# Kernel tuning notes

Measured on AMD Instinct MI355X. Metric: run time of the kernel, lower is better.

## Reference

```python
import jax, jax.numpy as jnp
import numpy as np

B, OBS, NH, LAT = 8192, 256, 2048, 128

def setup_inputs() -> dict:
    key = jax.random.key(0)
    k1, k2, k3, k4, k5, k6 = jax.random.split(key, 6)
    s1 = 1.0 / np.sqrt(OBS + NH)
    s2 = 1.0 / np.sqrt(NH)
    return {
        "x": jax.random.normal(k1, (B, OBS), dtype=jnp.float32),
        "h": jax.random.normal(k2, (B, NH), dtype=jnp.float32),
        "W_i2h": jax.random.normal(k3, (NH, OBS + NH), dtype=jnp.float32) * s1,
        "b_i2h": jax.random.normal(k4, (NH,), dtype=jnp.float32) * s1,
        "W_h2o": jax.random.normal(k5, (2 * LAT, NH), dtype=jnp.float32) * s2,
        "b_h2o": jax.random.normal(k6, (2 * LAT,), dtype=jnp.float32) * s2,
    }

def reference(x, h, W_i2h, b_i2h, W_h2o, b_h2o):
    # combined = cat((x, h), dim=1)  -> [B, OBS+NH]
    combined = jnp.concatenate([x, h], axis=1)
    # h_new = tanh(i2h(combined));  Linear is y = x @ W.T + b
    h_new = jnp.tanh(combined @ W_i2h.T + b_i2h)
    out = h_new @ W_h2o.T + b_h2o  # [B, 2*LAT]
    return (out, h_new)
```

## Files before the change

### kernel.cpp

```cpp
#include <hip/hip_runtime.h>
#include <hip/hip_bf16.h>
#include <cstdint>

using bf16 = __hip_bfloat16;
typedef __attribute__((ext_vector_type(8))) short short8;
typedef __attribute__((ext_vector_type(4))) float floatx4;

static constexpr int BATCH = 8192;
static constexpr int K1    = 2304;
static constexpr int N1    = 2048;
static constexpr int K2    = 2048;
static constexpr int N2    = 256;

__device__ __forceinline__ void gload_lds16(const void* g, void* l) {
  __builtin_amdgcn_global_load_lds(
      (const __attribute__((address_space(1))) void*)g,
      (__attribute__((address_space(3))) void*)l, 16, 0, 0);
}

__device__ __forceinline__ float fast_tanh(float x) {
  float e = __builtin_amdgcn_exp2f(x * 2.8853900817779268f);
  return 1.0f - 2.0f * __builtin_amdgcn_rcpf(e + 1.0f);
}

__device__ __forceinline__ short8 cvt8(const float* src) {
  float4 a = ((const float4*)src)[0];
  float4 b = ((const float4*)src)[1];
  union { short8 v; bf16 e[8]; } u;
  u.e[0] = __float2bfloat16(a.x); u.e[1] = __float2bfloat16(a.y);
  u.e[2] = __float2bfloat16(a.z); u.e[3] = __float2bfloat16(a.w);
  u.e[4] = __float2bfloat16(b.x); u.e[5] = __float2bfloat16(b.y);
  u.e[6] = __float2bfloat16(b.z); u.e[7] = __float2bfloat16(b.w);
  return u.v;
}

static constexpr int SEG0 = BATCH * (K1 / 8);
static constexpr int SEG1 = N1 * K1 / 8;
static constexpr int SEG2 = N2 * K2 / 8;
__global__ __launch_bounds__(256) void prep(
    const float* __restrict__ x, const float* __restrict__ h,
    const float* __restrict__ W1, const float* __restrict__ W2,
    bf16* __restrict__ comb, bf16* __restrict__ W1b, bf16* __restrict__ W2b) {
  int i = blockIdx.x * 256 + threadIdx.x;
  if (i < SEG0) {
    int row  = i / 288;
    int slot = i - row * 288;
    const float* src = (slot < 32) ? (x + (size_t)row * 256 + slot * 8)
                                   : (h + (size_t)row * 2048 + (slot - 32) * 8);
    *(short8*)(comb + (size_t)row * 2304 + slot * 8) = cvt8(src);
  } else if (i < SEG0 + SEG1) {
    int j = i - SEG0;
    *(short8*)(W1b + (size_t)j * 8) = cvt8(W1 + (size_t)j * 8);
  } else {
    int j = i - (SEG0 + SEG1);
    *(short8*)(W2b + (size_t)j * 8) = cvt8(W2 + (size_t)j * 8);
  }
}

__global__ __launch_bounds__(256) void bias_init(
    const float* __restrict__ bias, float* __restrict__ out) {
  int i = blockIdx.x * 256 + threadIdx.x;
  float4 b = ((const float4*)bias)[i & 63];
  ((float4*)out)[i] = b;
}

__global__ __launch_bounds__(256) void gemm1_tanh(
    const bf16* __restrict__ A, const bf16* __restrict__ W,
    const float* __restrict__ bias,
    float* __restrict__ hf32, bf16* __restrict__ hb16) {
  __shared__ bf16 As[128 * 64];
  __shared__ bf16 Bs[128 * 64];
  const int t    = threadIdx.x;
  const int lane = t & 63;
  const int wave = t >> 6;
  const int wm   = (wave & 1) * 64;
  const int wn   = (wave >> 1) * 64;
  const int quad = lane >> 4;
  const int r15  = lane & 15;
  const int srow = t >> 3;
  const int sc   = t & 7;

  const size_t Abase = (size_t)blockIdx.x * 128 * K1;
  const size_t Bbase = (size_t)blockIdx.y * 128 * K1;

  floatx4 acc[4][4];
  const floatx4 z = {0.f, 0.f, 0.f, 0.f};
#pragma unroll
  for (int i = 0; i < 4; i++)
#pragma unroll
    for (int j = 0; j < 4; j++) acc[i][j] = z;

  for (int kt = 0; kt < K1 / 64; ++kt) {
    const int k0 = kt * 64;
    __syncthreads();
#pragma unroll
    for (int it = 0; it < 4; ++it) {
      int row = it * 32 + srow;
      int gc  = k0 + ((sc ^ (row & 7)) << 3);
      gload_lds16(A + Abase + (size_t)row * K1 + gc,
                  (char*)As + it * 4096 + t * 16);
    }
#pragma unroll
    for (int it = 0; it < 4; ++it) {
      int row = it * 32 + srow;
      int gc  = k0 + ((sc ^ (row & 7)) << 3);
      gload_lds16(W + Bbase + (size_t)row * K1 + gc,
                  (char*)Bs + it * 4096 + t * 16);
    }
    __syncthreads();
#pragma unroll
    for (int ks = 0; ks < 2; ++ks) {
      short8 af[4], bfr[4];
      const int kq = ks * 4 + quad;
#pragma unroll
      for (int mt = 0; mt < 4; ++mt) {
        int row = wm + mt * 16 + r15;
        af[mt] = *(const short8*)((const char*)As + row * 128 +
                                  ((kq ^ (row & 7)) << 4));
      }
#pragma unroll
      for (int nt = 0; nt < 4; ++nt) {
        int row = wn + nt * 16 + r15;
        bfr[nt] = *(const short8*)((const char*)Bs + row * 128 +
                                   ((kq ^ (row & 7)) << 4));
      }
#pragma unroll
      for (int mt = 0; mt < 4; ++mt)
#pragma unroll
        for (int nt = 0; nt < 4; ++nt)
          acc[mt][nt] = __builtin_amdgcn_mfma_f32_16x16x32_bf16(
              af[mt], bfr[nt], acc[mt][nt], 0, 0, 0);
    }
  }

  const int gcol0 = blockIdx.y * 128 + wn;
  float bv[4];
#pragma unroll
  for (int nt = 0; nt < 4; ++nt) bv[nt] = bias[gcol0 + nt * 16 + r15];
  const size_t grow0 = (size_t)blockIdx.x * 128 + wm;
#pragma unroll
  for (int mt = 0; mt < 4; ++mt) {
#pragma unroll
    for (int i = 0; i < 4; ++i) {
      size_t gr = grow0 + mt * 16 + quad * 4 + i;
      size_t rb = gr * (size_t)N1;
#pragma unroll
      for (int nt = 0; nt < 4; ++nt) {
        int gc = gcol0 + nt * 16 + r15;
        float v = fast_tanh(acc[mt][nt][i] + bv[nt]);
        hf32[rb + gc] = v;
        hb16[rb + gc] = __float2bfloat16(v);
      }
    }
  }
}

__global__ __launch_bounds__(256) void gemm2_out(
    const bf16* __restrict__ A, const bf16* __restrict__ W,
    float* __restrict__ out) {
  __shared__ bf16 As[32 * 64];
  __shared__ bf16 Bs[256 * 64];
  const int t    = threadIdx.x;
  const int lane = t & 63;
  const int wave = t >> 6;
  const int quad = lane >> 4;
  const int r15  = lane & 15;
  const int srow = t >> 3;
  const int sc   = t & 7;

  const int mrow0 = blockIdx.x * 32;
  const int kbase = blockIdx.y * (K2 / 2);

  floatx4 acc[2][4];
  const floatx4 z = {0.f, 0.f, 0.f, 0.f};
#pragma unroll
  for (int i = 0; i < 2; i++)
#pragma unroll
    for (int j = 0; j < 4; j++) acc[i][j] = z;

  for (int kt = 0; kt < 16; ++kt) {
    const int k0 = kbase + kt * 64;
    __syncthreads();
    {
      int row = srow;
      int gc  = k0 + ((sc ^ (row & 7)) << 3);
      gload_lds16(A + (size_t)(mrow0 + row) * K2 + gc, (char*)As + t * 16);
    }
#pragma unroll
    for (int it = 0; it < 8; ++it) {
      int row = it * 32 + srow;
      int gc  = k0 + ((sc ^ (row & 7)) << 3);
      gload_lds16(W + (size_t)row * K2 + gc,
                  (char*)Bs + it * 4096 + t * 16);
    }
    __syncthreads();
#pragma unroll
    for (int ks = 0; ks < 2; ++ks) {
      short8 af[2], bfr[4];
      const int kq = ks * 4 + quad;
#pragma unroll
      for (int mt = 0; mt < 2; ++mt) {
        int row = mt * 16 + r15;
        af[mt] = *(const short8*)((const char*)As + row * 128 +
                                  ((kq ^ (row & 7)) << 4));
      }
#pragma unroll
      for (int nt = 0; nt < 4; ++nt) {
        int row = wave * 64 + nt * 16 + r15;
        bfr[nt] = *(const short8*)((const char*)Bs + row * 128 +
                                   ((kq ^ (row & 7)) << 4));
      }
#pragma unroll
      for (int mt = 0; mt < 2; ++mt)
#pragma unroll
        for (int nt = 0; nt < 4; ++nt)
          acc[mt][nt] = __builtin_amdgcn_mfma_f32_16x16x32_bf16(
              af[mt], bfr[nt], acc[mt][nt], 0, 0, 0);
    }
  }

  const int gcol0 = wave * 64;
#pragma unroll
  for (int mt = 0; mt < 2; ++mt) {
#pragma unroll
    for (int i = 0; i < 4; ++i) {
      size_t gr = (size_t)mrow0 + mt * 16 + quad * 4 + i;
      size_t rb = gr * (size_t)N2;
#pragma unroll
      for (int nt = 0; nt < 4; ++nt) {
        int gc = gcol0 + nt * 16 + r15;
        unsafeAtomicAdd(&out[rb + gc], acc[mt][nt][i]);
      }
    }
  }
}

extern "C" void kernel_launch(void* const* d_in, const int* in_sizes, int n_in,
                              void* d_out, int out_size, void* d_ws,
                              size_t ws_size, hipStream_t stream) {
  const float* x     = (const float*)d_in[0];
  const float* h     = (const float*)d_in[1];
  const float* W_i2h = (const float*)d_in[2];
  const float* b_i2h = (const float*)d_in[3];
  const float* W_h2o = (const float*)d_in[4];
  const float* b_h2o = (const float*)d_in[5];

  float* out       = (float*)d_out;
  float* hnew_f32  = out + (size_t)BATCH * N2;

  bf16* comb   = (bf16*)d_ws;
  bf16* Wi2h_b = comb + (size_t)BATCH * K1;
  bf16* Wh2o_b = Wi2h_b + (size_t)N1 * K1;
  bf16* hnew_b = Wh2o_b + (size_t)N2 * K2;

  bias_init<<<(BATCH * N2 / 4) / 256, 256, 0, stream>>>(b_h2o, out);

  prep<<<(SEG0 + SEG1 + SEG2) / 256, 256, 0, stream>>>(
      x, h, W_i2h, W_h2o, comb, Wi2h_b, Wh2o_b);

  gemm1_tanh<<<dim3(BATCH / 128, N1 / 128), 256, 0, stream>>>(
      comb, Wi2h_b, b_i2h, hnew_f32, hnew_b);

  gemm2_out<<<dim3(BATCH / 32, 2), 256, 0, stream>>>(hnew_b, Wh2o_b, out);
}
```

Baseline: 276.9 us.

## Fuse bias init into prep, swizzle GEMM1 tile order, split GEMM2 K four ways

New measurement: 290.8 us. 1.05x slower.

```diff
diff --git a/kernel.cpp b/kernel.cpp
--- a/kernel.cpp
+++ b/kernel.cpp
@@ -37,10 +37,13 @@
 static constexpr int SEG0 = BATCH * (K1 / 8);
 static constexpr int SEG1 = N1 * K1 / 8;
 static constexpr int SEG2 = N2 * K2 / 8;
+static constexpr int SEG3 = BATCH * N2 / 4;
 __global__ __launch_bounds__(256) void prep(
     const float* __restrict__ x, const float* __restrict__ h,
     const float* __restrict__ W1, const float* __restrict__ W2,
-    bf16* __restrict__ comb, bf16* __restrict__ W1b, bf16* __restrict__ W2b) {
+    const float* __restrict__ b2,
+    bf16* __restrict__ comb, bf16* __restrict__ W1b, bf16* __restrict__ W2b,
+    float* __restrict__ out) {
   int i = blockIdx.x * 256 + threadIdx.x;
   if (i < SEG0) {
     int row  = i / 288;
@@ -51,17 +54,13 @@
   } else if (i < SEG0 + SEG1) {
     int j = i - SEG0;
     *(short8*)(W1b + (size_t)j * 8) = cvt8(W1 + (size_t)j * 8);
-  } else {
+  } else if (i < SEG0 + SEG1 + SEG2) {
     int j = i - (SEG0 + SEG1);
     *(short8*)(W2b + (size_t)j * 8) = cvt8(W2 + (size_t)j * 8);
-  }
-}
-
-__global__ __launch_bounds__(256) void bias_init(
-    const float* __restrict__ bias, float* __restrict__ out) {
-  int i = blockIdx.x * 256 + threadIdx.x;
-  float4 b = ((const float4*)bias)[i & 63];
-  ((float4*)out)[i] = b;
+  } else {
+    int j = i - (SEG0 + SEG1 + SEG2);
+    ((float4*)out)[j] = ((const float4*)b2)[j & 63];
+  }
 }
 
 __global__ __launch_bounds__(256) void gemm1_tanh(
@@ -80,8 +79,14 @@
   const int srow = t >> 3;
   const int sc   = t & 7;
 
-  const size_t Abase = (size_t)blockIdx.x * 128 * K1;
-  const size_t Bbase = (size_t)blockIdx.y * 128 * K1;
+  const int lin    = blockIdx.y * 64 + blockIdx.x;
+  const int within = lin & 15;
+  const int st     = lin >> 4;
+  const int bm     = (st & 15) * 4 + (within & 3);
+  const int bn     = (st >> 4) * 4 + (within >> 2);
+
+  const size_t Abase = (size_t)bm * 128 * K1;
+  const size_t Bbase = (size_t)bn * 128 * K1;
 
   floatx4 acc[4][4];
   const floatx4 z = {0.f, 0.f, 0.f, 0.f};
@@ -133,11 +138,11 @@
     }
   }
 
-  const int gcol0 = blockIdx.y * 128 + wn;
+  const int gcol0 = bn * 128 + wn;
   float bv[4];
 #pragma unroll
   for (int nt = 0; nt < 4; ++nt) bv[nt] = bias[gcol0 + nt * 16 + r15];
-  const size_t grow0 = (size_t)blockIdx.x * 128 + wm;
+  const size_t grow0 = (size_t)bm * 128 + wm;
 #pragma unroll
   for (int mt = 0; mt < 4; ++mt) {
 #pragma unroll
@@ -169,7 +174,7 @@
   const int sc   = t & 7;
 
   const int mrow0 = blockIdx.x * 32;
-  const int kbase = blockIdx.y * (K2 / 2);
+  const int kbase = blockIdx.y * (K2 / 4);
 
   floatx4 acc[2][4];
   const floatx4 z = {0.f, 0.f, 0.f, 0.f};
@@ -178,7 +183,7 @@
 #pragma unroll
     for (int j = 0; j < 4; j++) acc[i][j] = z;
 
-  for (int kt = 0; kt < 16; ++kt) {
+  for (int kt = 0; kt < 8; ++kt) {
     const int k0 = kbase + kt * 64;
     __syncthreads();
     {
@@ -253,13 +258,11 @@
   bf16* Wh2o_b = Wi2h_b + (size_t)N1 * K1;
   bf16* hnew_b = Wh2o_b + (size_t)N2 * K2;
 
-  bias_init<<<(BATCH * N2 / 4) / 256, 256, 0, stream>>>(b_h2o, out);
-
-  prep<<<(SEG0 + SEG1 + SEG2) / 256, 256, 0, stream>>>(
-      x, h, W_i2h, W_h2o, comb, Wi2h_b, Wh2o_b);
+  prep<<<(SEG0 + SEG1 + SEG2 + SEG3) / 256, 256, 0, stream>>>(
+      x, h, W_i2h, W_h2o, b_h2o, comb, Wi2h_b, Wh2o_b, out);
 
   gemm1_tanh<<<dim3(BATCH / 128, N1 / 128), 256, 0, stream>>>(
       comb, Wi2h_b, b_i2h, hnew_f32, hnew_b);
 
-  gemm2_out<<<dim3(BATCH / 32, 2), 256, 0, stream>>>(hnew_b, Wh2o_b, out);
-}
+  gemm2_out<<<dim3(BATCH / 32, 4), 256, 0, stream>>>(hnew_b, Wh2o_b, out);
+}
```
